# Performance work log

Measured on AMD Instinct MI355X. Metric: run time of the kernel, lower is better.

The kernel has to match this reference:

```python
import jax, jax.numpy as jnp
import numpy as np

N_NODES = 50000
N_EDGES = 600000
F_IN = 128
H = 128
NUM_GRAPHS = 64
SELF_LOOP_W = 2.0  # improved=True


def setup_inputs() -> dict:
    key = jax.random.key(0)
    ks = jax.random.split(key, 16)
    x = jax.random.normal(ks[0], (N_NODES, F_IN), dtype=jnp.float32)
    edge_index = jax.random.randint(ks[1], (2, N_EDGES), 0, N_NODES, dtype=jnp.int64)
    batch_index = jnp.sort(jax.random.randint(ks[2], (N_NODES,), 0, NUM_GRAPHS, dtype=jnp.int64))
    edge_weight = jax.random.uniform(ks[3], (N_EDGES,), dtype=jnp.float32)
    def lin(k, fin, fout):
        s = 1.0 / np.sqrt(fin)
        kw, kb = jax.random.split(k)
        W = jax.random.uniform(kw, (fin, fout), minval=-s, maxval=s, dtype=jnp.float32)
        b = jax.random.uniform(kb, (fout,), minval=-s, maxval=s, dtype=jnp.float32)
        return W, b
    W0, b0 = lin(ks[4], F_IN, H)
    W1, b1 = lin(ks[5], H, H)
    W2, b2 = lin(ks[6], H, H)
    W3, b3 = lin(ks[7], H, H)
    Wout, bout = lin(ks[8], 2 * H, 1)
    return dict(x=x, edge_index=edge_index, batch_index=batch_index, edge_weight=edge_weight,
                W0=W0, b0=b0, W1=W1, b1=b1, W2=W2, b2=b2, W3=W3, b3=b3, Wout=Wout, bout=bout)


def reference(x, edge_index, batch_index, edge_weight, W0, b0, W1, b1, W2, b2, W3, b3, Wout, bout):
    N = x.shape[0]
    loop = jnp.arange(N)
    src = jnp.concatenate([edge_index[0], loop])  # [E+N]
    dst = jnp.concatenate([edge_index[1], loop])
    w = jnp.concatenate([edge_weight, jnp.full((N,), SELF_LOOP_W, dtype=x.dtype)])
    # symmetric GCN normalization: deg over destination, norm = d^-1/2[src]*w*d^-1/2[dst]
    deg = jax.ops.segment_sum(w, dst, num_segments=N)
    dinv = jnp.where(deg > 0, jax.lax.rsqrt(deg), 0.0)
    norm = dinv[src] * w * dinv[dst]  # [E+N]

    def conv(h, W, b):
        h = h @ W  # dense transform before aggregation
        msg = h[src] * norm[:, None]
        return jax.ops.segment_sum(msg, dst, num_segments=N) + b

    h = jnp.tanh(conv(x, W0, b0))
    h = jnp.tanh(conv(h, W1, b1))
    h = jnp.tanh(conv(h, W2, b2))
    h = jnp.tanh(conv(h, W3, b3))

    gmax = jax.ops.segment_max(h, batch_index, num_segments=NUM_GRAPHS)
    gmax = jnp.where(jnp.isfinite(gmax), gmax, 0.0)  # guard empty graphs
    cnt = jax.ops.segment_sum(jnp.ones((N,), dtype=h.dtype), batch_index, num_segments=NUM_GRAPHS)
    gmean = jax.ops.segment_sum(h, batch_index, num_segments=NUM_GRAPHS) / jnp.maximum(cnt, 1.0)[:, None]
    hidden = jnp.concatenate([gmax, gmean], axis=1)  # [B, 2H]
    out = hidden @ Wout + bout  # [B, 1]
    return out, hidden
```

## Files before the change

kernel.cpp:

```cpp
#include <hip/hip_runtime.h>
#include <hip/hip_bf16.h>
#include <hip/hip_fp16.h>

typedef __hip_bfloat16 bf16;
typedef _Float16 half8 __attribute__((ext_vector_type(8)));
typedef float f32x4 __attribute__((ext_vector_type(4)));

#define FDIM 128
#define SELF_W 2.0f
#define NGRAPH 64
#define DEG_SCALE 1048576.0f
#define DEG_MASK  ((1ull<<44) - 1ull)

__device__ __forceinline__ float b2f(bf16 v){ return __bfloat162float(v); }

__device__ __forceinline__ unsigned fenc(float f){
  unsigned b = __float_as_uint(f);
  return (b & 0x80000000u) ? ~b : (b | 0x80000000u);
}
__device__ __forceinline__ float fdec(unsigned u){
  unsigned b = (u & 0x80000000u) ? (u ^ 0x80000000u) : ~u;
  return __uint_as_float(b);
}

__device__ __forceinline__ float rdf(const void* p, long long i, int f32){
  return f32 ? ((const float*)p)[i] : b2f(((const bf16*)p)[i]);
}
__device__ __forceinline__ int rdi(const void* p, long long i, int i64){
  return i64 ? (int)(((const long long*)p)[i]) : ((const int*)p)[i];
}

__global__ __launch_bounds__(256) void k_probe(const unsigned short* __restrict__ x16,
                                               const int* __restrict__ ei32,
                                               int* __restrict__ flags){
  __shared__ int cbig, codd;
  int tid = threadIdx.x;
  if (tid == 0){ cbig = 0; codd = 0; }
  __syncthreads();
  for (int i = tid; i < 4096; i += 256){
    int e = (x16[i] >> 7) & 0xFF;
    if (e >= 134) atomicAdd(&cbig, 1);
  }
  for (int i = tid; i < 512; i += 256){
    if (ei32[2*i + 1] != 0) atomicAdd(&codd, 1);
  }
  __syncthreads();
  if (tid == 0){
    flags[0] = (cbig >= 64) ? 1 : 0;
    flags[1] = (codd < 8)  ? 1 : 0;
  }
}

struct PtrPack { const void* p[10]; };
__global__ void k_cvt_params(PtrPack pk, float* __restrict__ pf,
                             _Float16* __restrict__ wt,
                             const int* __restrict__ flags){
  const int sz[10]  = {16384,16384,16384,16384,128,128,128,128,256,1};
  const int dst[10] = {0,16384,32768,49152,65536,65664,65792,65920,66048,66304};
  int i = blockIdx.x*blockDim.x + threadIdx.x;
  if (i >= 66305) return;
  int seg = 0, rem = i;
  while (rem >= sz[seg]){ rem -= sz[seg]; seg++; }
  float v = rdf(pk.p[seg], rem, flags[0]);
  pf[dst[seg] + rem] = v;
  if (seg < 4){
    int k = rem >> 7, n = rem & 127;
    wt[seg*16384 + n*128 + k] = (_Float16)v;
  }
}

__global__ void k_packed_init(unsigned long long* packed, int N){
  int i = blockIdx.x*blockDim.x + threadIdx.x;
  if (i < N) packed[i] = (unsigned long long)(SELF_W * DEG_SCALE);
}

__global__ void k_edge_deg(const void* __restrict__ ei, const void* __restrict__ ew,
                           unsigned long long* __restrict__ packed,
                           unsigned* __restrict__ rank, unsigned* __restrict__ epk,
                           int E, unsigned Epad, int N, const int* __restrict__ flags){
  int e = blockIdx.x*blockDim.x + threadIdx.x;
  if ((unsigned)e < Epad) epk[e] = 0u;
  if (e >= E) return;
  int d = rdi(ei, (long long)E + e, flags[1]);
  unsigned r = 0u;
  if ((unsigned)d < (unsigned)N){
    float w = rdf(ew, e, flags[0]);
    unsigned long long add = (1ull << 44) |
        (unsigned long long)__float2uint_rn(w * DEG_SCALE);
    unsigned long long old = atomicAdd(&packed[d], add);
    r = (unsigned)(old >> 44);
  }
  rank[e] = r;
}

__device__ __forceinline__ unsigned wave_incl_scan(unsigned v){
  int lane = threadIdx.x & 63;
  #pragma unroll
  for (int d = 1; d < 64; d <<= 1){
    unsigned t = __shfl_up(v, d, 64);
    if (lane >= d) v += t;
  }
  return v;
}

__global__ __launch_bounds__(256) void k_scan_pre(const unsigned long long* __restrict__ packed,
                                                  float* __restrict__ dinv,
                                                  unsigned* __restrict__ bsum, int N){
  __shared__ unsigned wsh[4];
  int tid = threadIdx.x, lane = tid & 63, wid = tid >> 6;
  int i0 = blockIdx.x*1024 + tid*4;
  unsigned tsum = 0u;
  #pragma unroll
  for (int j = 0; j < 4; j++){
    int i = i0 + j;
    if (i < N){
      unsigned long long pv = packed[i];
      tsum += ((unsigned)(pv >> 44) + 7u) & ~7u;
      float d = (float)(pv & DEG_MASK) * (1.0f / DEG_SCALE);
      dinv[i] = (d > 0.f) ? rsqrtf(d) : 0.f;
    }
  }
  #pragma unroll
  for (int d = 1; d < 64; d <<= 1) tsum += __shfl_down(tsum, d, 64);
  if (lane == 0) wsh[wid] = tsum;
  __syncthreads();
  if (tid == 0) bsum[blockIdx.x] = wsh[0] + wsh[1] + wsh[2] + wsh[3];
}

__global__ __launch_bounds__(64) void k_scan_mid(unsigned* __restrict__ bsum,
                                                 unsigned* __restrict__ off,
                                                 int nb, int N){
  int lane = threadIdx.x;
  unsigned v = (lane < nb) ? bsum[lane] : 0u;
  unsigned isc = wave_incl_scan(v);
  if (lane < nb) bsum[lane] = isc - v;
  if (lane == 63) off[N] = isc;
}

__global__ __launch_bounds__(256) void k_scan_fin(const unsigned long long* __restrict__ packed,
                                                  const unsigned* __restrict__ bsum,
                                                  unsigned* __restrict__ off, int N){
  __shared__ unsigned wsh[4];
  int tid = threadIdx.x, lane = tid & 63, wid = tid >> 6;
  int i0 = blockIdx.x*1024 + tid*4;
  unsigned v0=0u,v1=0u,v2=0u,v3=0u;
  if (i0+0 < N) v0 = ((unsigned)(packed[i0+0] >> 44) + 7u) & ~7u;
  if (i0+1 < N) v1 = ((unsigned)(packed[i0+1] >> 44) + 7u) & ~7u;
  if (i0+2 < N) v2 = ((unsigned)(packed[i0+2] >> 44) + 7u) & ~7u;
  if (i0+3 < N) v3 = ((unsigned)(packed[i0+3] >> 44) + 7u) & ~7u;
  unsigned tsum = v0+v1+v2+v3;
  unsigned isc = wave_incl_scan(tsum);
  if (lane == 63) wsh[wid] = isc;
  __syncthreads();
  unsigned wbase = 0u;
  #pragma unroll
  for (int w = 0; w < 4; w++) if (w < wid) wbase += wsh[w];
  unsigned ex = bsum[blockIdx.x] + wbase + (isc - tsum);
  if (i0+0 < N) off[i0+0] = ex;
  if (i0+1 < N) off[i0+1] = ex + v0;
  if (i0+2 < N) off[i0+2] = ex + v0 + v1;
  if (i0+3 < N) off[i0+3] = ex + v0 + v1 + v2;
}

__global__ void k_bucket(const void* __restrict__ ei, const void* __restrict__ ew,
                         const float* __restrict__ dinv,
                         const unsigned* __restrict__ off,
                         const unsigned* __restrict__ rank,
                         unsigned* __restrict__ epk,
                         int E, unsigned Epad, int N, const int* __restrict__ flags){
  int e = blockIdx.x*blockDim.x + threadIdx.x;
  if (e >= E) return;
  int s_ = rdi(ei, e, flags[1]);
  int d  = rdi(ei, (long long)E + e, flags[1]);
  if ((unsigned)s_ >= (unsigned)N || (unsigned)d >= (unsigned)N) return;
  unsigned pos = off[d] + rank[e];
  if (pos < Epad){
    float coef = dinv[s_] * rdf(ew, e, flags[0]) * dinv[d];
    _Float16 ch = (_Float16)coef;
    unsigned cu = (unsigned)__builtin_bit_cast(unsigned short, ch);
    epk[pos] = ((unsigned)s_ & 0xffffu) | (cu << 16);
  }
}

__global__ void k_bounds(const void* __restrict__ bat, int N,
                         unsigned* __restrict__ start, unsigned* __restrict__ gcnt,
                         const int* __restrict__ flags){
  __shared__ unsigned s[NGRAPH+1];
  int g = threadIdx.x;
  int i64 = flags[1];
  if (g <= NGRAPH){
    int lo = 0, hi = N;
    while (lo < hi){ int mid = (lo + hi) >> 1; if (rdi(bat, mid, i64) < g) lo = mid + 1; else hi = mid; }
    s[g] = (unsigned)lo;
  }
  __syncthreads();
  if (g < NGRAPH){ start[g] = s[g]; gcnt[g] = s[g+1] - s[g]; }
  if (g == NGRAPH) start[NGRAPH] = s[NGRAPH];
}

template<int MODE>
__global__ __launch_bounds__(256) void k_gemm(const void* __restrict__ in,
                                              const _Float16* __restrict__ WT,
                                              _Float16* __restrict__ outp, int N,
                                              size_t pstride,
                                              const int* __restrict__ flags){
  __shared__ _Float16 sout[4*16*136];
  int tid  = threadIdx.x;
  int wid  = tid >> 6, lane = tid & 63;
  int ln   = lane & 15, quad = lane >> 4;
  int row0 = blockIdx.x * 64;
  int rowA = row0 + wid*16 + ln;
  int rA   = (rowA < N) ? rowA : (N > 0 ? N-1 : 0);

  half8 af[4];
  if (MODE == 1){
    const _Float16* src = (const _Float16*)in;
    #pragma unroll
    for (int kc = 0; kc < 4; kc++)
      af[kc] = *(const half8*)(src + (size_t)kc*pstride + (size_t)rA*32 + quad*8);
  } else {
    if (flags[0]){
      const float* src = (const float*)in + (size_t)rA*FDIM + quad*8;
      #pragma unroll
      for (int kc = 0; kc < 4; kc++){
        float4 a = *(const float4*)(src + kc*32);
        float4 b = *(const float4*)(src + kc*32 + 4);
        half8 h; h[0]=(_Float16)a.x; h[1]=(_Float16)a.y; h[2]=(_Float16)a.z; h[3]=(_Float16)a.w;
        h[4]=(_Float16)b.x; h[5]=(_Float16)b.y; h[6]=(_Float16)b.z; h[7]=(_Float16)b.w;
        af[kc] = h;
      }
    } else {
      const unsigned short* src = (const unsigned short*)in + (size_t)rA*FDIM + quad*8;
      #pragma unroll
      for (int kc = 0; kc < 4; kc++){
        ushort4 u0 = *(const ushort4*)(src + kc*32);
        ushort4 u1 = *(const ushort4*)(src + kc*32 + 4);
        half8 h;
        h[0]=(_Float16)__uint_as_float((unsigned)u0.x<<16);
        h[1]=(_Float16)__uint_as_float((unsigned)u0.y<<16);
        h[2]=(_Float16)__uint_as_float((unsigned)u0.z<<16);
        h[3]=(_Float16)__uint_as_float((unsigned)u0.w<<16);
        h[4]=(_Float16)__uint_as_float((unsigned)u1.x<<16);
        h[5]=(_Float16)__uint_as_float((unsigned)u1.y<<16);
        h[6]=(_Float16)__uint_as_float((unsigned)u1.z<<16);
        h[7]=(_Float16)__uint_as_float((unsigned)u1.w<<16);
        af[kc] = h;
      }
    }
  }

  f32x4 acc[8];
  #pragma unroll
  for (int nt = 0; nt < 8; nt++) acc[nt] = (f32x4){0.f,0.f,0.f,0.f};

  #pragma unroll
  for (int kc = 0; kc < 4; kc++){
    #pragma unroll
    for (int nt = 0; nt < 8; nt++){
      half8 bf = *(const half8*)(WT + (size_t)(nt*16 + ln)*FDIM + kc*32 + quad*8);
      acc[nt] = __builtin_amdgcn_mfma_f32_16x16x32_f16(af[kc], bf, acc[nt], 0, 0, 0);
    }
  }

  _Float16* so = sout + wid*2176;
  #pragma unroll
  for (int nt = 0; nt < 8; nt++)
    #pragma unroll
    for (int reg = 0; reg < 4; reg++)
      so[(quad*4 + reg)*136 + nt*16 + ln] = (_Float16)acc[nt][reg];
  __syncthreads();

  #pragma unroll
  for (int c = 0; c < 4; c++){
    int chunk = tid + c*256;
    int r = chunk >> 4, co = (chunk & 15)*8;
    int row = row0 + r;
    if (row < N){
      half8 v = *(const half8*)(sout + (r>>4)*2176 + (r&15)*136 + co);
      *(half8*)(outp + (size_t)(co>>5)*pstride + (size_t)row*32 + (co & 31)) = v;
    }
  }
}

__global__ __launch_bounds__(256) void k_agg(const _Float16* __restrict__ tp,
                                             const float* __restrict__ dinv,
                                             const unsigned* __restrict__ off,
                                             const unsigned* __restrict__ epk,
                                             const float* __restrict__ bias,
                                             _Float16* __restrict__ hp,
                                             int N, size_t pstride){
  int tid  = threadIdx.x;
  int wv   = tid >> 6, lane = tid & 63;
  int quad = lane >> 4, ql = lane & 15;
  int panel = blockIdx.x & 3;
  int n = (blockIdx.x >> 2)*16 + wv*4 + quad;
  bool valid = (n < N);
  int nn = valid ? n : 0;
  const _Float16* tpp = tp + (size_t)panel*pstride;
  const _Float16* myt = tpp + ql*2;

  float di = dinv[nn];
  float sw = di * di * SELF_W;
  float2 sv = __half22float2(*(const __half2*)(myt + (size_t)nn*32));
  float a0 = sw * sv.x, a1 = sw * sv.y;
  float b0 = 0.f, b1 = 0.f;

  unsigned beg = off[nn];
  unsigned end = valid ? off[nn+1] : beg;
  for (unsigned i = beg; i < end; i += 8){
    uint4 p0 = *(const uint4*)(epk + i);
    uint4 p1 = *(const uint4*)(epk + i + 4);
    unsigned vs[8] = {p0.x,p0.y,p0.z,p0.w,p1.x,p1.y,p1.z,p1.w};
    __half2 tv[8];
    #pragma unroll
    for (int j = 0; j < 8; j++)
      tv[j] = *(const __half2*)(myt + (size_t)(vs[j] & 0xffffu)*32);
    #pragma unroll
    for (int j = 0; j < 8; j++){
      float w = (float)__builtin_bit_cast(_Float16, (unsigned short)(vs[j] >> 16));
      float2 tf = __half22float2(tv[j]);
      if (j & 1){ b0 += w * tf.x; b1 += w * tf.y; }
      else      { a0 += w * tf.x; a1 += w * tf.y; }
    }
  }
  a0 += b0; a1 += b1;
  int cc = panel*32 + ql*2;
  a0 = tanhf(a0 + bias[cc]);
  a1 = tanhf(a1 + bias[cc+1]);
  if (valid)
    *(__half2*)(hp + (size_t)panel*pstride + (size_t)n*32 + ql*2) = __floats2half2_rn(a0, a1);
}

__global__ void k_pool_init(unsigned* gmaxu, float* gsum){
  int i = blockIdx.x*blockDim.x + threadIdx.x;
  if (i < NGRAPH*FDIM){ gmaxu[i] = 0u; gsum[i] = 0.f; }
}

__global__ __launch_bounds__(256) void k_pool2(const _Float16* __restrict__ hp,
                                               const unsigned* __restrict__ start,
                                               unsigned* __restrict__ gmaxu,
                                               float* __restrict__ gsum,
                                               size_t pstride){
  int g = blockIdx.x >> 2, sub = blockIdx.x & 3;
  int col = threadIdx.x & 127, half_ = threadIdx.x >> 7;
  const _Float16* hpp = hp + (size_t)(col >> 5)*pstride + (col & 31);
  unsigned s0 = start[g], s1 = start[g+1];
  float m = -INFINITY, sm = 0.f;
  for (unsigned n = s0 + sub*2 + half_; n < s1; n += 8){
    float v = (float)hpp[(size_t)n*32];
    m = fmaxf(m, v); sm += v;
  }
  __shared__ float shm[256], shs[256];
  shm[threadIdx.x] = m; shs[threadIdx.x] = sm;
  __syncthreads();
  if (half_ == 0){
    m = fmaxf(m, shm[threadIdx.x + 128]);
    sm += shs[threadIdx.x + 128];
    if (m > -INFINITY) atomicMax(&gmaxu[g*FDIM + col], fenc(m));
    atomicAdd(&gsum[g*FDIM + col], sm);
  }
}

__global__ __launch_bounds__(256) void k_out(const unsigned* __restrict__ gmaxu,
                                             const float* __restrict__ gsum,
                                             const unsigned* __restrict__ gcnt,
                                             const float* __restrict__ Wout,
                                             const float* __restrict__ bout,
                                             void* __restrict__ outp,
                                             const int* __restrict__ flags){
  int g = blockIdx.x;
  int c = threadIdx.x;
  unsigned nc = gcnt[g];
  float val;
  if (c < FDIM){
    val = nc ? fdec(gmaxu[g*FDIM + c]) : 0.f;
  } else {
    float denom = nc ? (float)nc : 1.f;
    val = gsum[g*FDIM + (c - FDIM)] / denom;
  }
  int f32out = flags[0];
  int hidx = NGRAPH + g*(2*FDIM) + c;
  if (f32out) ((float*)outp)[hidx] = val;
  else        ((bf16*)outp)[hidx] = __float2bfloat16(val);

  __shared__ float red[256];
  red[c] = val * Wout[c];
  __syncthreads();
  for (int s = 128; s > 0; s >>= 1){
    if (c < s) red[c] += red[c + s];
    __syncthreads();
  }
  if (c == 0){
    float o = red[0] + bout[0];
    if (f32out) ((float*)outp)[g] = o;
    else        ((bf16*)outp)[g] = __float2bfloat16(o);
  }
}

extern "C" void kernel_launch(void* const* d_in, const int* in_sizes, int n_in,
                              void* d_out, int out_size, void* d_ws, size_t ws_size,
                              hipStream_t stream){
  int N = in_sizes[0] / FDIM;
  int E = in_sizes[3];
  int NB = (N + 1023) / 1024;
  unsigned Epad = (unsigned)E + 8u*(unsigned)N;
  size_t pstride = (size_t)N * 32;

  char* p = (char*)d_ws;
  auto alloc = [&](size_t bytes){ char* r = p; p += (bytes + 255) & ~(size_t)255; return r; };
  int*       flags  = (int*)      alloc(16);
  float*     pf     = (float*)    alloc((size_t)(66305 + 64)*4);
  _Float16*  wt     = (_Float16*) alloc((size_t)4*FDIM*FDIM*2);
  unsigned long long* packed = (unsigned long long*)alloc((size_t)N*8);
  float*     dinv   = (float*)    alloc((size_t)N*4);
  unsigned*  off    = (unsigned*) alloc((size_t)(N+1)*4);
  unsigned*  bsum   = (unsigned*) alloc((size_t)128*4);
  unsigned*  rank   = (unsigned*) alloc((size_t)E*4);
  unsigned*  epk    = (unsigned*) alloc((size_t)Epad*4);
  _Float16*  th     = (_Float16*) alloc((size_t)N*FDIM*2);
  _Float16*  hh     = (_Float16*) alloc((size_t)N*FDIM*2);
  unsigned*  gmaxu  = (unsigned*) alloc((size_t)NGRAPH*FDIM*4);
  float*     gsum   = (float*)    alloc((size_t)NGRAPH*FDIM*4);
  unsigned*  gcnt   = (unsigned*) alloc((size_t)NGRAPH*4);
  unsigned*  gstart = (unsigned*) alloc((size_t)(NGRAPH+1)*4);

  float* bf_[4] = {pf + 65536, pf + 65664, pf + 65792, pf + 65920};
  float* Woutf  = pf + 66048;
  float* boutf  = pf + 66304;

  k_probe<<<1, 256, 0, stream>>>((const unsigned short*)d_in[0], (const int*)d_in[1], flags);

  int gE = (E + 255)/256, gN = (N + 255)/256;
  int gEp = ((int)Epad + 255)/256;
  PtrPack pk;
  pk.p[0]=d_in[4]; pk.p[1]=d_in[6]; pk.p[2]=d_in[8]; pk.p[3]=d_in[10];
  pk.p[4]=d_in[5]; pk.p[5]=d_in[7]; pk.p[6]=d_in[9]; pk.p[7]=d_in[11];
  pk.p[8]=d_in[12]; pk.p[9]=d_in[13];
  k_cvt_params<<<(66305 + 255)/256, 256, 0, stream>>>(pk, pf, wt, flags);
  k_packed_init<<<gN, 256, 0, stream>>>(packed, N);
  k_edge_deg<<<gEp, 256, 0, stream>>>(d_in[1], d_in[3], packed, rank, epk, E, Epad, N, flags);
  k_scan_pre<<<NB, 256, 0, stream>>>(packed, dinv, bsum, N);
  k_scan_mid<<<1, 64, 0, stream>>>(bsum, off, NB, N);
  k_scan_fin<<<NB, 256, 0, stream>>>(packed, bsum, off, N);
  k_bucket<<<gE, 256, 0, stream>>>(d_in[1], d_in[3], dinv, off, rank, epk, E, Epad, N, flags);
  k_bounds<<<1, 128, 0, stream>>>(d_in[2], N, gstart, gcnt, flags);

  int gG = (N + 63)/64;
  int gA = ((N + 15)/16)*4;

  k_gemm<0><<<gG, 256, 0, stream>>>(d_in[0], wt + 0*16384, th, N, pstride, flags);
  k_agg<<<gA, 256, 0, stream>>>(th, dinv, off, epk, bf_[0], hh, N, pstride);
  for (int l = 1; l < 4; l++){
    k_gemm<1><<<gG, 256, 0, stream>>>(hh, wt + (size_t)l*16384, th, N, pstride, flags);
    k_agg<<<gA, 256, 0, stream>>>(th, dinv, off, epk, bf_[l], hh, N, pstride);
  }

  k_pool_init<<<(NGRAPH*FDIM + 255)/256, 256, 0, stream>>>(gmaxu, gsum);
  k_pool2<<<4*NGRAPH, 256, 0, stream>>>(hh, gstart, gmaxu, gsum, pstride);
  k_out<<<NGRAPH, 256, 0, stream>>>(gmaxu, gsum, gcnt, Woutf, boutf, d_out, flags);
}
```

Measured before the change: 408.7 us.

## Fuse setup and pooling kernels, precompute self-loop weight, use fast tanh

Merges the parameter conversion, degree-buffer init and graph-boundary search into one setup kernel, and moves edge-buffer zeroing into the scan kernel. Pooling, mean/max finalisation and the output projection are fused into one atomic-free kernel with one block per graph. The aggregation kernel reads a precomputed self-loop weight and uses an exp/reciprocal tanh. This cuts launch count and atomics, but pooling now has fewer blocks, zeroing runs on a small grid, and the tanh approximation slightly changes numerics.

```diff
diff --git a/kernel.cpp b/kernel.cpp
--- a/kernel.cpp
+++ b/kernel.cpp
@@ -14,20 +14,18 @@
 
 __device__ __forceinline__ float b2f(bf16 v){ return __bfloat162float(v); }
 
-__device__ __forceinline__ unsigned fenc(float f){
-  unsigned b = __float_as_uint(f);
-  return (b & 0x80000000u) ? ~b : (b | 0x80000000u);
-}
-__device__ __forceinline__ float fdec(unsigned u){
-  unsigned b = (u & 0x80000000u) ? (u ^ 0x80000000u) : ~u;
-  return __uint_as_float(b);
-}
-
 __device__ __forceinline__ float rdf(const void* p, long long i, int f32){
   return f32 ? ((const float*)p)[i] : b2f(((const bf16*)p)[i]);
 }
 __device__ __forceinline__ int rdi(const void* p, long long i, int i64){
   return i64 ? (int)(((const long long*)p)[i]) : ((const int*)p)[i];
+}
+
+__device__ __forceinline__ float tanh_fast(float x){
+  float ax = fabsf(x);
+  float e  = __expf(-2.0f*ax);
+  float r  = (1.0f - e) * __builtin_amdgcn_rcpf(1.0f + e);
+  return copysignf(r, x);
 }
 
 __global__ __launch_bounds__(256) void k_probe(const unsigned short* __restrict__ x16,
@@ -52,34 +50,47 @@
 }
 
 struct PtrPack { const void* p[10]; };
-__global__ void k_cvt_params(PtrPack pk, float* __restrict__ pf,
-                             _Float16* __restrict__ wt,
-                             const int* __restrict__ flags){
+__global__ __launch_bounds__(256) void k_setup(PtrPack pk, float* __restrict__ pf,
+                                               _Float16* __restrict__ wt,
+                                               unsigned long long* __restrict__ packed,
+                                               const void* __restrict__ bat,
+                                               unsigned* __restrict__ gstart,
+                                               int N, const int* __restrict__ flags){
   const int sz[10]  = {16384,16384,16384,16384,128,128,128,128,256,1};
   const int dst[10] = {0,16384,32768,49152,65536,65664,65792,65920,66048,66304};
   int i = blockIdx.x*blockDim.x + threadIdx.x;
-  if (i >= 66305) return;
-  int seg = 0, rem = i;
-  while (rem >= sz[seg]){ rem -= sz[seg]; seg++; }
-  float v = rdf(pk.p[seg], rem, flags[0]);
-  pf[dst[seg] + rem] = v;
-  if (seg < 4){
-    int k = rem >> 7, n = rem & 127;
-    wt[seg*16384 + n*128 + k] = (_Float16)v;
-  }
-}
-
-__global__ void k_packed_init(unsigned long long* packed, int N){
-  int i = blockIdx.x*blockDim.x + threadIdx.x;
-  if (i < N) packed[i] = (unsigned long long)(SELF_W * DEG_SCALE);
+  if (i < 66305){
+    int seg = 0, rem = i;
+    while (rem >= sz[seg]){ rem -= sz[seg]; seg++; }
+    float v = rdf(pk.p[seg], rem, flags[0]);
+    pf[dst[seg] + rem] = v;
+    if (seg < 4){
+      int k = rem >> 7, n = rem & 127;
+      wt[seg*16384 + n*128 + k] = (_Float16)v;
+    }
+  }
+  int stride = gridDim.x*blockDim.x;
+  for (int j = i; j < N; j += stride)
+    packed[j] = (unsigned long long)(SELF_W * DEG_SCALE);
+  if (blockIdx.x == gridDim.x - 1){
+    __shared__ unsigned s[NGRAPH+1];
+    int g = threadIdx.x;
+    int i64 = flags[1];
+    if (g <= NGRAPH){
+      int lo = 0, hi = N;
+      while (lo < hi){ int mid = (lo + hi) >> 1; if (rdi(bat, mid, i64) < g) lo = mid + 1; else hi = mid; }
+      s[g] = (unsigned)lo;
+    }
+    __syncthreads();
+    if (g <= NGRAPH) gstart[g] = s[g];
+  }
 }
 
 __global__ void k_edge_deg(const void* __restrict__ ei, const void* __restrict__ ew,
                            unsigned long long* __restrict__ packed,
-                           unsigned* __restrict__ rank, unsigned* __restrict__ epk,
-                           int E, unsigned Epad, int N, const int* __restrict__ flags){
+                           unsigned* __restrict__ rank,
+                           int E, int N, const int* __restrict__ flags){
   int e = blockIdx.x*blockDim.x + threadIdx.x;
-  if ((unsigned)e < Epad) epk[e] = 0u;
   if (e >= E) return;
   int d = rdi(ei, (long long)E + e, flags[1]);
   unsigned r = 0u;
@@ -105,9 +116,14 @@
 
 __global__ __launch_bounds__(256) void k_scan_pre(const unsigned long long* __restrict__ packed,
                                                   float* __restrict__ dinv,
-                                                  unsigned* __restrict__ bsum, int N){
+                                                  float* __restrict__ swv,
+                                                  unsigned* __restrict__ bsum,
+                                                  unsigned* __restrict__ epk, unsigned Epad,
+                                                  int N){
   __shared__ unsigned wsh[4];
   int tid = threadIdx.x, lane = tid & 63, wid = tid >> 6;
+  unsigned gid = blockIdx.x*blockDim.x + tid, gstr = gridDim.x*blockDim.x;
+  for (unsigned j = gid; j < Epad; j += gstr) epk[j] = 0u;
   int i0 = blockIdx.x*1024 + tid*4;
   unsigned tsum = 0u;
   #pragma unroll
@@ -117,7 +133,9 @@
       unsigned long long pv = packed[i];
       tsum += ((unsigned)(pv >> 44) + 7u) & ~7u;
       float d = (float)(pv & DEG_MASK) * (1.0f / DEG_SCALE);
-      dinv[i] = (d > 0.f) ? rsqrtf(d) : 0.f;
+      float di = (d > 0.f) ? rsqrtf(d) : 0.f;
+      dinv[i] = di;
+      swv[i]  = di * di * SELF_W;
     }
   }
   #pragma unroll
@@ -180,22 +198,6 @@
     unsigned cu = (unsigned)__builtin_bit_cast(unsigned short, ch);
     epk[pos] = ((unsigned)s_ & 0xffffu) | (cu << 16);
   }
-}
-
-__global__ void k_bounds(const void* __restrict__ bat, int N,
-                         unsigned* __restrict__ start, unsigned* __restrict__ gcnt,
-                         const int* __restrict__ flags){
-  __shared__ unsigned s[NGRAPH+1];
-  int g = threadIdx.x;
-  int i64 = flags[1];
-  if (g <= NGRAPH){
-    int lo = 0, hi = N;
-    while (lo < hi){ int mid = (lo + hi) >> 1; if (rdi(bat, mid, i64) < g) lo = mid + 1; else hi = mid; }
-    s[g] = (unsigned)lo;
-  }
-  __syncthreads();
-  if (g < NGRAPH){ start[g] = s[g]; gcnt[g] = s[g+1] - s[g]; }
-  if (g == NGRAPH) start[NGRAPH] = s[NGRAPH];
 }
 
 template<int MODE>
@@ -283,7 +285,7 @@
 }
 
 __global__ __launch_bounds__(256) void k_agg(const _Float16* __restrict__ tp,
-                                             const float* __restrict__ dinv,
+                                             const float* __restrict__ swv,
                                              const unsigned* __restrict__ off,
                                              const unsigned* __restrict__ epk,
                                              const float* __restrict__ bias,
@@ -299,8 +301,7 @@
   const _Float16* tpp = tp + (size_t)panel*pstride;
   const _Float16* myt = tpp + ql*2;
 
-  float di = dinv[nn];
-  float sw = di * di * SELF_W;
+  float sw = swv[nn];
   float2 sv = __half22float2(*(const __half2*)(myt + (size_t)nn*32));
   float a0 = sw * sv.x, a1 = sw * sv.y;
   float b0 = 0.f, b1 = 0.f;
@@ -325,72 +326,54 @@
   }
   a0 += b0; a1 += b1;
   int cc = panel*32 + ql*2;
-  a0 = tanhf(a0 + bias[cc]);
-  a1 = tanhf(a1 + bias[cc+1]);
+  a0 = tanh_fast(a0 + bias[cc]);
+  a1 = tanh_fast(a1 + bias[cc+1]);
   if (valid)
     *(__half2*)(hp + (size_t)panel*pstride + (size_t)n*32 + ql*2) = __floats2half2_rn(a0, a1);
 }
 
-__global__ void k_pool_init(unsigned* gmaxu, float* gsum){
-  int i = blockIdx.x*blockDim.x + threadIdx.x;
-  if (i < NGRAPH*FDIM){ gmaxu[i] = 0u; gsum[i] = 0.f; }
-}
-
-__global__ __launch_bounds__(256) void k_pool2(const _Float16* __restrict__ hp,
-                                               const unsigned* __restrict__ start,
-                                               unsigned* __restrict__ gmaxu,
-                                               float* __restrict__ gsum,
-                                               size_t pstride){
-  int g = blockIdx.x >> 2, sub = blockIdx.x & 3;
-  int col = threadIdx.x & 127, half_ = threadIdx.x >> 7;
+__global__ __launch_bounds__(256) void k_pool_out(const _Float16* __restrict__ hp,
+                                                  const unsigned* __restrict__ gstart,
+                                                  const float* __restrict__ Wout,
+                                                  const float* __restrict__ bout,
+                                                  void* __restrict__ outp,
+                                                  size_t pstride,
+                                                  const int* __restrict__ flags){
+  int g = blockIdx.x, tid = threadIdx.x;
+  int col = tid & 127, sub = tid >> 7;
   const _Float16* hpp = hp + (size_t)(col >> 5)*pstride + (col & 31);
-  unsigned s0 = start[g], s1 = start[g+1];
+  unsigned s0 = gstart[g], s1 = gstart[g+1];
   float m = -INFINITY, sm = 0.f;
-  for (unsigned n = s0 + sub*2 + half_; n < s1; n += 8){
+  for (unsigned n = s0 + sub; n < s1; n += 2){
     float v = (float)hpp[(size_t)n*32];
     m = fmaxf(m, v); sm += v;
   }
   __shared__ float shm[256], shs[256];
-  shm[threadIdx.x] = m; shs[threadIdx.x] = sm;
-  __syncthreads();
-  if (half_ == 0){
-    m = fmaxf(m, shm[threadIdx.x + 128]);
-    sm += shs[threadIdx.x + 128];
-    if (m > -INFINITY) atomicMax(&gmaxu[g*FDIM + col], fenc(m));
-    atomicAdd(&gsum[g*FDIM + col], sm);
-  }
-}
-
-__global__ __launch_bounds__(256) void k_out(const unsigned* __restrict__ gmaxu,
-                                             const float* __restrict__ gsum,
-                                             const unsigned* __restrict__ gcnt,
-                                             const float* __restrict__ Wout,
-                                             const float* __restrict__ bout,
-                                             void* __restrict__ outp,
-                                             const int* __restrict__ flags){
-  int g = blockIdx.x;
-  int c = threadIdx.x;
-  unsigned nc = gcnt[g];
+  shm[tid] = m; shs[tid] = sm;
+  __syncthreads();
+  unsigned cnt = s1 - s0;
   float val;
-  if (c < FDIM){
-    val = nc ? fdec(gmaxu[g*FDIM + c]) : 0.f;
+  if (sub == 0){
+    float mm = fmaxf(shm[tid], shm[tid + 128]);
+    val = (cnt > 0 && mm > -INFINITY) ? mm : 0.f;
   } else {
-    float denom = nc ? (float)nc : 1.f;
-    val = gsum[g*FDIM + (c - FDIM)] / denom;
-  }
+    float ss = shs[tid] + shs[tid - 128];
+    val = ss / (float)(cnt ? cnt : 1u);
+  }
+  int hcol = (sub == 0) ? col : (128 + col);
   int f32out = flags[0];
-  int hidx = NGRAPH + g*(2*FDIM) + c;
+  int hidx = NGRAPH + g*(2*FDIM) + hcol;
   if (f32out) ((float*)outp)[hidx] = val;
   else        ((bf16*)outp)[hidx] = __float2bfloat16(val);
 
   __shared__ float red[256];
-  red[c] = val * Wout[c];
+  red[hcol] = val * Wout[hcol];
   __syncthreads();
   for (int s = 128; s > 0; s >>= 1){
-    if (c < s) red[c] += red[c + s];
+    if (tid < s) red[tid] += red[tid + s];
     __syncthreads();
   }
-  if (c == 0){
+  if (tid == 0){
     float o = red[0] + bout[0];
     if (f32out) ((float*)outp)[g] = o;
     else        ((bf16*)outp)[g] = __float2bfloat16(o);
@@ -413,15 +396,13 @@
   _Float16*  wt     = (_Float16*) alloc((size_t)4*FDIM*FDIM*2);
   unsigned long long* packed = (unsigned long long*)alloc((size_t)N*8);
   float*     dinv   = (float*)    alloc((size_t)N*4);
+  float*     swv    = (float*)    alloc((size_t)N*4);
   unsigned*  off    = (unsigned*) alloc((size_t)(N+1)*4);
   unsigned*  bsum   = (unsigned*) alloc((size_t)128*4);
   unsigned*  rank   = (unsigned*) alloc((size_t)E*4);
   unsigned*  epk    = (unsigned*) alloc((size_t)Epad*4);
   _Float16*  th     = (_Float16*) alloc((size_t)N*FDIM*2);
   _Float16*  hh     = (_Float16*) alloc((size_t)N*FDIM*2);
-  unsigned*  gmaxu  = (unsigned*) alloc((size_t)NGRAPH*FDIM*4);
-  float*     gsum   = (float*)    alloc((size_t)NGRAPH*FDIM*4);
-  unsigned*  gcnt   = (unsigned*) alloc((size_t)NGRAPH*4);
   unsigned*  gstart = (unsigned*) alloc((size_t)(NGRAPH+1)*4);
 
   float* bf_[4] = {pf + 65536, pf + 65664, pf + 65792, pf + 65920};
@@ -430,32 +411,27 @@
 
   k_probe<<<1, 256, 0, stream>>>((const unsigned short*)d_in[0], (const int*)d_in[1], flags);
 
-  int gE = (E + 255)/256, gN = (N + 255)/256;
-  int gEp = ((int)Epad + 255)/256;
+  int gE = (E + 255)/256;
   PtrPack pk;
   pk.p[0]=d_in[4]; pk.p[1]=d_in[6]; pk.p[2]=d_in[8]; pk.p[3]=d_in[10];
   pk.p[4]=d_in[5]; pk.p[5]=d_in[7]; pk.p[6]=d_in[9]; pk.p[7]=d_in[11];
   pk.p[8]=d_in[12]; pk.p[9]=d_in[13];
-  k_cvt_params<<<(66305 + 255)/256, 256, 0, stream>>>(pk, pf, wt, flags);
-  k_packed_init<<<gN, 256, 0, stream>>>(packed, N);
-  k_edge_deg<<<gEp, 256, 0, stream>>>(d_in[1], d_in[3], packed, rank, epk, E, Epad, N, flags);
-  k_scan_pre<<<NB, 256, 0, stream>>>(packed, dinv, bsum, N);
+  k_setup<<<(66305 + 255)/256, 256, 0, stream>>>(pk, pf, wt, packed, d_in[2], gstart, N, flags);
+  k_edge_deg<<<gE, 256, 0, stream>>>(d_in[1], d_in[3], packed, rank, E, N, flags);
+  k_scan_pre<<<NB, 256, 0, stream>>>(packed, dinv, swv, bsum, epk, Epad, N);
   k_scan_mid<<<1, 64, 0, stream>>>(bsum, off, NB, N);
   k_scan_fin<<<NB, 256, 0, stream>>>(packed, bsum, off, N);
   k_bucket<<<gE, 256, 0, stream>>>(d_in[1], d_in[3], dinv, off, rank, epk, E, Epad, N, flags);
-  k_bounds<<<1, 128, 0, stream>>>(d_in[2], N, gstart, gcnt, flags);
 
   int gG = (N + 63)/64;
   int gA = ((N + 15)/16)*4;
 
   k_gemm<0><<<gG, 256, 0, stream>>>(d_in[0], wt + 0*16384, th, N, pstride, flags);
-  k_agg<<<gA, 256, 0, stream>>>(th, dinv, off, epk, bf_[0], hh, N, pstride);
+  k_agg<<<gA, 256, 0, stream>>>(th, swv, off, epk, bf_[0], hh, N, pstride);
   for (int l = 1; l < 4; l++){
     k_gemm<1><<<gG, 256, 0, stream>>>(hh, wt + (size_t)l*16384, th, N, pstride, flags);
-    k_agg<<<gA, 256, 0, stream>>>(th, dinv, off, epk, bf_[l], hh, N, pstride);
-  }
-
-  k_pool_init<<<(NGRAPH*FDIM + 255)/256, 256, 0, stream>>>(gmaxu, gsum);
-  k_pool2<<<4*NGRAPH, 256, 0, stream>>>(hh, gstart, gmaxu, gsum, pstride);
-  k_out<<<NGRAPH, 256, 0, stream>>>(gmaxu, gsum, gcnt, Woutf, boutf, d_out, flags);
-}
+    k_agg<<<gA, 256, 0, stream>>>(th, swv, off, epk, bf_[l], hh, N, pstride);
+  }
+
+  k_pool_out<<<NGRAPH, 256, 0, stream>>>(hh, gstart, Woutf, boutf, d_out, pstride, flags);
+}
```

After: 495.7 us. 1.21x slower.
